# Performance work log

Measured on AMD Instinct MI355X. Metric: run time of the kernel, lower is better.

Reference implementation:

```python
import jax, jax.numpy as jnp
import numpy as np

N_NODES = 100000
N_EDGES = 1600000
D_NODE = 32
D_EDGE = 16
D_OUT = 32
L2_EPS = 1e-12  # tf.math.l2_normalize default epsilon


def setup_inputs() -> dict:
    key = jax.random.key(0)
    k_h, k_e, k_w, k_s, k_d = jax.random.split(key, 5)
    h = jax.random.normal(k_h, (N_NODES, D_NODE), dtype=jnp.float32)
    e = jax.random.normal(k_e, (N_EDGES, D_EDGE), dtype=jnp.float32)
    # Dense(output_dim) kernel over concat(node, edge) features
    W = jax.random.normal(k_w, (D_NODE + D_EDGE, D_OUT), dtype=jnp.float32) * 0.1
    b = jnp.zeros((D_OUT,), dtype=jnp.float32)
    src = jax.random.randint(k_s, (N_EDGES,), 0, N_NODES, dtype=jnp.int32)
    dst = jax.random.randint(k_d, (N_EDGES,), 0, N_NODES, dtype=jnp.int32)
    return {"h": h, "e": e, "W": W, "b": b, "src": src, "dst": dst}


def reference(h, e, W, b, src, dst):
    # message: m = concat(h[src], e)              [E, D+De]
    # reduce:  new_h = mean over (self_msg, mailbox) of Dense(msg)
    # Dense is affine (activation=None), so Dense(mean) == mean(Dense): one GEMM.
    n = h.shape[0]
    msg = jnp.concatenate([h[src], e], axis=-1)                      # [E, D+De]
    agg = jax.ops.segment_sum(msg, dst, num_segments=n)              # [N, D+De]
    deg = jax.ops.segment_sum(jnp.ones_like(dst, dtype=h.dtype), dst, num_segments=n)
    self_msg = jnp.concatenate([h, jnp.zeros((n, e.shape[1]), h.dtype)], axis=-1)
    mean_msg = (self_msg + agg) / (deg[:, None] + 1.0)               # self counts in the mean
    new_h = mean_msg @ W + b                                         # [N, D_OUT]
    # activation=None -> identity; then tf.math.l2_normalize(axis=-1)
    sq = jnp.sum(new_h * new_h, axis=-1, keepdims=True)
    return new_h * jax.lax.rsqrt(jnp.maximum(sq, L2_EPS))
```

## Files before the change

kernel.cpp:

```cpp
#include <hip/hip_runtime.h>

#define D_NODE 32
#define D_EDGE 16
#define D_IN   48
#define D_OUT  32
#define L2_EPS 1e-12f

#define NPB       64
#define BKT_SHIFT 6
#define MAX_NB    4096
#define CH        8192
#define CTH       1024
#define EPT       (CH / CTH)
#define ATH       256
#define CAP       2048
#define KPT       (CAP / ATH)


__global__ __launch_bounds__(CTH) void k_count(
    const int* __restrict__ dst, int* __restrict__ cnt, int n_edges, int nb)
{
    extern __shared__ int c[];
    for (int i = threadIdx.x; i < nb; i += CTH) c[i] = 0;
    __syncthreads();
    int base = blockIdx.x * CH + threadIdx.x;
    #pragma unroll
    for (int k = 0; k < EPT; ++k) {
        int i = base + k * CTH;
        if (i < n_edges) atomicAdd(&c[dst[i] >> BKT_SHIFT], 1);
    }
    __syncthreads();
    for (int i = threadIdx.x; i < nb; i += CTH)
        if (c[i]) atomicAdd(&cnt[i], c[i]);
}

__global__ __launch_bounds__(1024) void k_offs2(
    const int* __restrict__ cnt, int* __restrict__ offsets,
    int* __restrict__ cursor, int nb)
{
    __shared__ int s[1024];
    const int PT = MAX_NB / 1024;
    int t = threadIdx.x;
    int tot[PT];
    int ts = 0;
    #pragma unroll
    for (int j = 0; j < PT; ++j) {
        int b = t * PT + j;
        tot[j] = (b < nb) ? cnt[b] : 0;
        ts += tot[j];
    }
    s[t] = ts;
    __syncthreads();
    for (int off = 1; off < 1024; off <<= 1) {
        int u = (t >= off) ? s[t - off] : 0;
        __syncthreads();
        s[t] += u;
        __syncthreads();
    }
    if (t == 1023) offsets[nb] = s[1023];
    int run = s[t] - ts;
    #pragma unroll
    for (int j = 0; j < PT; ++j) {
        int b = t * PT + j;
        if (b < nb) { offsets[b] = run; cursor[b] = run; run += tot[j]; }
    }
}

__global__ __launch_bounds__(CTH) void k_scatter3(
    const int* __restrict__ dst, const int* __restrict__ src,
    int* __restrict__ cursor, int2* __restrict__ meta2, int n_edges, int nb)
{
    extern __shared__ int sm[];
    int* lhist = sm;
    int* lbase = sm + nb;
    int* lrank = sm + 2 * nb;
    for (int i = threadIdx.x; i < nb; i += CTH) { lhist[i] = 0; lrank[i] = 0; }
    __syncthreads();
    int base = blockIdx.x * CH + threadIdx.x;
    int d[EPT];
    #pragma unroll
    for (int k = 0; k < EPT; ++k) {
        int i = base + k * CTH;
        if (i < n_edges) {
            d[k] = dst[i];
            atomicAdd(&lhist[d[k] >> BKT_SHIFT], 1);
        }
    }
    __syncthreads();
    for (int i = threadIdx.x; i < nb; i += CTH)
        if (lhist[i]) lbase[i] = atomicAdd(&cursor[i], lhist[i]);
    __syncthreads();
    #pragma unroll
    for (int k = 0; k < EPT; ++k) {
        int i = base + k * CTH;
        if (i < n_edges) {
            int bkt = d[k] >> BKT_SHIFT;
            int r = atomicAdd(&lrank[bkt], 1);
            meta2[lbase[bkt] + r] =
                make_int2(src[i] | ((d[k] & (NPB - 1)) << 20), i);
        }
    }
}

__global__ __launch_bounds__(ATH, 8) void k_accum(
    const float* __restrict__ h, const float4* __restrict__ e4,
    const float* __restrict__ W, const float* __restrict__ b,
    const int* __restrict__ offsets, const int2* __restrict__ meta2,
    float* __restrict__ out, int n_nodes)
{
    __shared__ float Ws[D_IN * D_OUT];
    __shared__ float bs[D_OUT];
    __shared__ int2 csr[CAP];
    __shared__ int cnt[NPB], cnt2[NPB], offs[NPB];

    for (int i = threadIdx.x; i < D_IN * D_OUT; i += ATH) Ws[i] = W[i];
    if (threadIdx.x < D_OUT) bs[threadIdx.x] = b[threadIdx.x];
    if (threadIdx.x < NPB) { cnt[threadIdx.x] = 0; cnt2[threadIdx.x] = 0; }
    __syncthreads();

    int g  = threadIdx.x >> 2;
    int jg = threadIdx.x & 3;

    float4 ha0 = make_float4(0.f, 0.f, 0.f, 0.f);
    float4 ha1 = make_float4(0.f, 0.f, 0.f, 0.f);
    float4 ea  = make_float4(0.f, 0.f, 0.f, 0.f);
    float deg = 0.f;

    int b0 = offsets[blockIdx.x], b1 = offsets[blockIdx.x + 1];

    for (int t0 = b0; t0 < b1; t0 += CAP) {
        int tn = min(CAP, b1 - t0);

        int2 m[KPT];
        #pragma unroll
        for (int k = 0; k < KPT; ++k) {
            int i = (int)threadIdx.x + k * ATH;
            if (i < tn) {
                m[k] = meta2[t0 + i];
                atomicAdd(&cnt[(m[k].x >> 20) & (NPB - 1)], 1);
            }
        }
        __syncthreads();

        if (threadIdx.x < 64) {
            int p = cnt[threadIdx.x];
            int x = p;
            #pragma unroll
            for (int o = 1; o < 64; o <<= 1) {
                int y = __shfl_up(x, o);
                if (threadIdx.x >= o) x += y;
            }
            offs[threadIdx.x] = x - p;
        }
        int myc = cnt[g];
        __syncthreads();

        #pragma unroll
        for (int k = 0; k < KPT; ++k) {
            int i = (int)threadIdx.x + k * ATH;
            if (i < tn) {
                int dl = (m[k].x >> 20) & (NPB - 1);
                int r = atomicAdd(&cnt2[dl], 1);
                csr[offs[dl] + r] = make_int2(m[k].x & 0xFFFFF, m[k].y);
            }
        }
        if (threadIdx.x < NPB) cnt[threadIdx.x] = 0;
        deg += (float)myc;
        __syncthreads();

        int mybase = offs[g];
        #pragma unroll 4
        for (int s = 0; s < myc; ++s) {
            int2 c = csr[mybase + s];
            const float4* hr = reinterpret_cast<const float4*>(
                h + (size_t)c.x * D_NODE) + 2 * jg;
            float4 h0 = hr[0], h1 = hr[1];
            float4 ev = e4[(size_t)c.y * 4 + jg];
            ha0.x += h0.x; ha0.y += h0.y; ha0.z += h0.z; ha0.w += h0.w;
            ha1.x += h1.x; ha1.y += h1.y; ha1.z += h1.z; ha1.w += h1.w;
            ea.x  += ev.x; ea.y  += ev.y; ea.z  += ev.z; ea.w  += ev.w;
        }
        if (threadIdx.x < NPB) cnt2[threadIdx.x] = 0;
        __syncthreads();
    }

    float (*mrow)[D_IN + 1] = reinterpret_cast<float (*)[D_IN + 1]>(csr);

    int node = blockIdx.x * NPB + g;
    if (node < n_nodes) {
        float inv = 1.f / (deg + 1.f);
        const float4* hs = reinterpret_cast<const float4*>(
            h + (size_t)node * D_NODE) + 2 * jg;
        float4 s0 = hs[0], s1 = hs[1];
        mrow[g][8 * jg + 0] = (ha0.x + s0.x) * inv;
        mrow[g][8 * jg + 1] = (ha0.y + s0.y) * inv;
        mrow[g][8 * jg + 2] = (ha0.z + s0.z) * inv;
        mrow[g][8 * jg + 3] = (ha0.w + s0.w) * inv;
        mrow[g][8 * jg + 4] = (ha1.x + s1.x) * inv;
        mrow[g][8 * jg + 5] = (ha1.y + s1.y) * inv;
        mrow[g][8 * jg + 6] = (ha1.z + s1.z) * inv;
        mrow[g][8 * jg + 7] = (ha1.w + s1.w) * inv;
        mrow[g][D_NODE + 4 * jg + 0] = ea.x * inv;
        mrow[g][D_NODE + 4 * jg + 1] = ea.y * inv;
        mrow[g][D_NODE + 4 * jg + 2] = ea.z * inv;
        mrow[g][D_NODE + 4 * jg + 3] = ea.w * inv;
    }
    __syncthreads();
    if (node >= n_nodes) return;

    const float* row = mrow[g];
    float a[8];
    #pragma unroll
    for (int q = 0; q < 8; ++q) a[q] = bs[jg * 8 + q];
    #pragma unroll
    for (int k = 0; k < D_IN; ++k) {
        float mk = row[k];
        const float* w = Ws + k * D_OUT + jg * 8;
        #pragma unroll
        for (int q = 0; q < 8; ++q) a[q] += mk * w[q];
    }
    float sq = 0.f;
    #pragma unroll
    for (int q = 0; q < 8; ++q) sq += a[q] * a[q];
    sq += __shfl_xor(sq, 1);
    sq += __shfl_xor(sq, 2);
    float r = rsqrtf(fmaxf(sq, L2_EPS));
    float4* o4 = reinterpret_cast<float4*>(out + (size_t)node * D_OUT) + 2 * jg;
    o4[0] = make_float4(a[0] * r, a[1] * r, a[2] * r, a[3] * r);
    o4[1] = make_float4(a[4] * r, a[5] * r, a[6] * r, a[7] * r);
}

__global__ __launch_bounds__(256) void scatter_kernel(
    const float* __restrict__ h, const float* __restrict__ e,
    const int* __restrict__ src, const int* __restrict__ dst,
    float* __restrict__ agg, float* __restrict__ deg, int n_edges)
{
    int tid  = blockIdx.x * blockDim.x + threadIdx.x;
    int edge = tid >> 4;
    int c    = tid & 15;
    if (edge >= n_edges) return;
    int s = src[edge], d = dst[edge];
    float v0 = h[(size_t)s * D_NODE + c];
    float v1 = h[(size_t)s * D_NODE + 16 + c];
    float v2 = e[(size_t)edge * D_EDGE + c];
    float* row = agg + (size_t)d * D_IN;
    atomicAdd(row + c, v0);
    atomicAdd(row + 16 + c, v1);
    atomicAdd(row + 32 + c, v2);
    if (c == 0) atomicAdd(deg + d, 1.0f);
}

__global__ __launch_bounds__(256) void node_kernel(
    const float* __restrict__ h, const float* __restrict__ W, const float* __restrict__ b,
    const float* __restrict__ agg, const float* __restrict__ deg,
    float* __restrict__ out, int n_nodes)
{
    __shared__ float Ws[D_IN * D_OUT];
    __shared__ float bs[D_OUT];
    for (int i = threadIdx.x; i < D_IN * D_OUT; i += blockDim.x) Ws[i] = W[i];
    if (threadIdx.x < D_OUT) bs[threadIdx.x] = b[threadIdx.x];
    __syncthreads();
    int node = blockIdx.x * blockDim.x + threadIdx.x;
    if (node >= n_nodes) return;
    const float4* h4 = reinterpret_cast<const float4*>(h + (size_t)node * D_NODE);
    const float4* a4 = reinterpret_cast<const float4*>(agg + (size_t)node * D_IN);
    float inv = 1.0f / (deg[node] + 1.0f);
    float m[D_IN];
    #pragma unroll
    for (int k = 0; k < D_NODE / 4; ++k) {
        float4 hv = h4[k]; float4 av = a4[k];
        m[4*k+0] = (hv.x + av.x) * inv; m[4*k+1] = (hv.y + av.y) * inv;
        m[4*k+2] = (hv.z + av.z) * inv; m[4*k+3] = (hv.w + av.w) * inv;
    }
    #pragma unroll
    for (int k = D_NODE / 4; k < D_IN / 4; ++k) {
        float4 av = a4[k];
        m[4*k+0] = av.x * inv; m[4*k+1] = av.y * inv;
        m[4*k+2] = av.z * inv; m[4*k+3] = av.w * inv;
    }
    float acc[D_OUT];
    #pragma unroll
    for (int j = 0; j < D_OUT; ++j) acc[j] = bs[j];
    #pragma unroll
    for (int k = 0; k < D_IN; ++k) {
        float mk = m[k];
        #pragma unroll
        for (int j = 0; j < D_OUT; ++j) acc[j] += mk * Ws[k * D_OUT + j];
    }
    float sq = 0.0f;
    #pragma unroll
    for (int j = 0; j < D_OUT; ++j) sq += acc[j] * acc[j];
    float r = rsqrtf(fmaxf(sq, L2_EPS));
    float4* o4 = reinterpret_cast<float4*>(out + (size_t)node * D_OUT);
    #pragma unroll
    for (int j = 0; j < D_OUT / 4; ++j) {
        float4 v;
        v.x = acc[4*j+0] * r; v.y = acc[4*j+1] * r;
        v.z = acc[4*j+2] * r; v.w = acc[4*j+3] * r;
        o4[j] = v;
    }
}

extern "C" void kernel_launch(void* const* d_in, const int* in_sizes, int n_in,
                              void* d_out, int out_size, void* d_ws, size_t ws_size,
                              hipStream_t stream) {
    const float* h   = (const float*)d_in[0];
    const float* e   = (const float*)d_in[1];
    const float* W   = (const float*)d_in[2];
    const float* b   = (const float*)d_in[3];
    const int*   src = (const int*)d_in[4];
    const int*   dst = (const int*)d_in[5];
    float* out = (float*)d_out;

    const int n_nodes = in_sizes[0] / D_NODE;
    const int n_edges = in_sizes[4];

    const int nb = (n_nodes + NPB - 1) / NPB;
    const int nc = (n_edges + CH - 1) / CH;

    size_t o_cnt     = 0;
    size_t o_offsets = o_cnt + nb;
    size_t o_cursor  = o_offsets + nb + 1;
    size_t o_meta2   = (o_cursor + (size_t)nb + 1) & ~(size_t)1;
    size_t need      = (o_meta2 + (size_t)n_edges * 2) * sizeof(int);

    if (nb <= MAX_NB && n_nodes < (1 << 20) && need <= ws_size && n_edges > 0) {
        int* ws_i    = (int*)d_ws;
        int* cnt     = ws_i + o_cnt;
        int* offsets = ws_i + o_offsets;
        int* cursor  = ws_i + o_cursor;
        int2* meta2  = (int2*)(ws_i + o_meta2);

        hipMemsetAsync(cnt, 0, (size_t)nb * sizeof(int), stream);
        k_count<<<nc, CTH, (size_t)nb * sizeof(int), stream>>>(
            dst, cnt, n_edges, nb);
        k_offs2<<<1, 1024, 0, stream>>>(cnt, offsets, cursor, nb);
        k_scatter3<<<nc, CTH, (size_t)3 * nb * sizeof(int), stream>>>(
            dst, src, cursor, meta2, n_edges, nb);
        k_accum<<<nb, ATH, 0, stream>>>(
            h, (const float4*)e, W, b, offsets, meta2, out, n_nodes);
    } else {
        float* agg = (float*)d_ws;
        float* deg = agg + (size_t)n_nodes * D_IN;
        hipMemsetAsync(d_ws, 0, (size_t)n_nodes * (D_IN + 1) * sizeof(float), stream);
        long long threads = (long long)n_edges * 16;
        scatter_kernel<<<(int)((threads + 255) / 256), 256, 0, stream>>>(h, e, src, dst, agg, deg, n_edges);
        node_kernel<<<(n_nodes + 255) / 256, 256, 0, stream>>>(h, W, b, agg, deg, out, n_nodes);
    }
}
```

Measured before the change: 116.2 us.

## Permute edge features into bucket order during scatter for contiguous reads

The scatter pass now copies each edge's 16-float feature row into a bucket-sorted buffer alongside a compact 4-byte meta word, rather than writing an (src,edge_id) pair. The accumulate kernel then reads edge features from that bucket-contiguous buffer instead of gathering them randomly from the original array. This swaps random 64-byte gathers for a streaming read, at the cost of an extra scattered 64-byte write per edge and about 100MB of extra workspace. The previous path is kept as a fallback when the workspace is too small.

```diff
diff --git a/kernel.cpp b/kernel.cpp
--- a/kernel.cpp
+++ b/kernel.cpp
@@ -66,7 +66,49 @@
     }
 }
 
-__global__ __launch_bounds__(CTH) void k_scatter3(
+__global__ __launch_bounds__(CTH) void k_scatter_p(
+    const int* __restrict__ dst, const int* __restrict__ src,
+    int* __restrict__ cursor, int* __restrict__ meta1,
+    float4* __restrict__ ep, const float4* __restrict__ e4,
+    int n_edges, int nb)
+{
+    extern __shared__ int sm[];
+    int* lhist = sm;
+    int* lbase = sm + nb;
+    int* lrank = sm + 2 * nb;
+    for (int i = threadIdx.x; i < nb; i += CTH) { lhist[i] = 0; lrank[i] = 0; }
+    __syncthreads();
+    int base = blockIdx.x * CH + threadIdx.x;
+    int d[EPT];
+    #pragma unroll
+    for (int k = 0; k < EPT; ++k) {
+        int i = base + k * CTH;
+        if (i < n_edges) {
+            d[k] = dst[i];
+            atomicAdd(&lhist[d[k] >> BKT_SHIFT], 1);
+        }
+    }
+    __syncthreads();
+    for (int i = threadIdx.x; i < nb; i += CTH)
+        if (lhist[i]) lbase[i] = atomicAdd(&cursor[i], lhist[i]);
+    __syncthreads();
+    #pragma unroll
+    for (int k = 0; k < EPT; ++k) {
+        int i = base + k * CTH;
+        if (i < n_edges) {
+            int bkt = d[k] >> BKT_SHIFT;
+            int r = atomicAdd(&lrank[bkt], 1);
+            int slot = lbase[bkt] + r;
+            meta1[slot] = src[i] | ((d[k] & (NPB - 1)) << 20);
+            const float4* er = e4 + (size_t)i * 4;
+            float4 v0 = er[0], v1 = er[1], v2 = er[2], v3 = er[3];
+            float4* wp = ep + (size_t)slot * 4;
+            wp[0] = v0; wp[1] = v1; wp[2] = v2; wp[3] = v3;
+        }
+    }
+}
+
+__global__ __launch_bounds__(CTH) void k_scatter_g(
     const int* __restrict__ dst, const int* __restrict__ src,
     int* __restrict__ cursor, int2* __restrict__ meta2, int n_edges, int nb)
 {
@@ -102,10 +144,10 @@
     }
 }
 
-__global__ __launch_bounds__(ATH, 8) void k_accum(
-    const float* __restrict__ h, const float4* __restrict__ e4,
+__global__ __launch_bounds__(ATH, 8) void k_accum_p(
+    const float* __restrict__ h, const float4* __restrict__ ep,
     const float* __restrict__ W, const float* __restrict__ b,
-    const int* __restrict__ offsets, const int2* __restrict__ meta2,
+    const int* __restrict__ offsets, const int* __restrict__ meta1,
     float* __restrict__ out, int n_nodes)
 {
     __shared__ float Ws[D_IN * D_OUT];
@@ -131,13 +173,13 @@
     for (int t0 = b0; t0 < b1; t0 += CAP) {
         int tn = min(CAP, b1 - t0);
 
-        int2 m[KPT];
+        int m[KPT];
         #pragma unroll
         for (int k = 0; k < KPT; ++k) {
             int i = (int)threadIdx.x + k * ATH;
             if (i < tn) {
-                m[k] = meta2[t0 + i];
-                atomicAdd(&cnt[(m[k].x >> 20) & (NPB - 1)], 1);
+                m[k] = meta1[t0 + i];
+                atomicAdd(&cnt[(m[k] >> 20) & (NPB - 1)], 1);
             }
         }
         __syncthreads();
@@ -159,9 +201,9 @@
         for (int k = 0; k < KPT; ++k) {
             int i = (int)threadIdx.x + k * ATH;
             if (i < tn) {
-                int dl = (m[k].x >> 20) & (NPB - 1);
+                int dl = (m[k] >> 20) & (NPB - 1);
                 int r = atomicAdd(&cnt2[dl], 1);
-                csr[offs[dl] + r] = make_int2(m[k].x & 0xFFFFF, m[k].y);
+                csr[offs[dl] + r] = make_int2(m[k] & 0xFFFFF, i);
             }
         }
         if (threadIdx.x < NPB) cnt[threadIdx.x] = 0;
@@ -175,7 +217,7 @@
             const float4* hr = reinterpret_cast<const float4*>(
                 h + (size_t)c.x * D_NODE) + 2 * jg;
             float4 h0 = hr[0], h1 = hr[1];
-            float4 ev = e4[(size_t)c.y * 4 + jg];
+            float4 ev = ep[(size_t)(t0 + c.y) * 4 + jg];
             ha0.x += h0.x; ha0.y += h0.y; ha0.z += h0.z; ha0.w += h0.w;
             ha1.x += h1.x; ha1.y += h1.y; ha1.z += h1.z; ha1.w += h1.w;
             ea.x  += ev.x; ea.y  += ev.y; ea.z  += ev.z; ea.w  += ev.w;
@@ -230,6 +272,134 @@
     o4[1] = make_float4(a[4] * r, a[5] * r, a[6] * r, a[7] * r);
 }
 
+__global__ __launch_bounds__(ATH, 8) void k_accum_g(
+    const float* __restrict__ h, const float4* __restrict__ e4,
+    const float* __restrict__ W, const float* __restrict__ b,
+    const int* __restrict__ offsets, const int2* __restrict__ meta2,
+    float* __restrict__ out, int n_nodes)
+{
+    __shared__ float Ws[D_IN * D_OUT];
+    __shared__ float bs[D_OUT];
+    __shared__ int2 csr[CAP];
+    __shared__ int cnt[NPB], cnt2[NPB], offs[NPB];
+
+    for (int i = threadIdx.x; i < D_IN * D_OUT; i += ATH) Ws[i] = W[i];
+    if (threadIdx.x < D_OUT) bs[threadIdx.x] = b[threadIdx.x];
+    if (threadIdx.x < NPB) { cnt[threadIdx.x] = 0; cnt2[threadIdx.x] = 0; }
+    __syncthreads();
+
+    int g  = threadIdx.x >> 2;
+    int jg = threadIdx.x & 3;
+
+    float4 ha0 = make_float4(0.f, 0.f, 0.f, 0.f);
+    float4 ha1 = make_float4(0.f, 0.f, 0.f, 0.f);
+    float4 ea  = make_float4(0.f, 0.f, 0.f, 0.f);
+    float deg = 0.f;
+
+    int b0 = offsets[blockIdx.x], b1 = offsets[blockIdx.x + 1];
+
+    for (int t0 = b0; t0 < b1; t0 += CAP) {
+        int tn = min(CAP, b1 - t0);
+
+        int2 m[KPT];
+        #pragma unroll
+        for (int k = 0; k < KPT; ++k) {
+            int i = (int)threadIdx.x + k * ATH;
+            if (i < tn) {
+                m[k] = meta2[t0 + i];
+                atomicAdd(&cnt[(m[k].x >> 20) & (NPB - 1)], 1);
+            }
+        }
+        __syncthreads();
+
+        if (threadIdx.x < 64) {
+            int p = cnt[threadIdx.x];
+            int x = p;
+            #pragma unroll
+            for (int o = 1; o < 64; o <<= 1) {
+                int y = __shfl_up(x, o);
+                if (threadIdx.x >= o) x += y;
+            }
+            offs[threadIdx.x] = x - p;
+        }
+        int myc = cnt[g];
+        __syncthreads();
+
+        #pragma unroll
+        for (int k = 0; k < KPT; ++k) {
+            int i = (int)threadIdx.x + k * ATH;
+            if (i < tn) {
+                int dl = (m[k].x >> 20) & (NPB - 1);
+                int r = atomicAdd(&cnt2[dl], 1);
+                csr[offs[dl] + r] = make_int2(m[k].x & 0xFFFFF, m[k].y);
+            }
+        }
+        if (threadIdx.x < NPB) cnt[threadIdx.x] = 0;
+        deg += (float)myc;
+        __syncthreads();
+
+        int mybase = offs[g];
+        #pragma unroll 4
+        for (int s = 0; s < myc; ++s) {
+            int2 c = csr[mybase + s];
+            const float4* hr = reinterpret_cast<const float4*>(
+                h + (size_t)c.x * D_NODE) + 2 * jg;
+            float4 h0 = hr[0], h1 = hr[1];
+            float4 ev = e4[(size_t)c.y * 4 + jg];
+            ha0.x += h0.x; ha0.y += h0.y; ha0.z += h0.z; ha0.w += h0.w;
+            ha1.x += h1.x; ha1.y += h1.y; ha1.z += h1.z; ha1.w += h1.w;
+            ea.x  += ev.x; ea.y  += ev.y; ea.z  += ev.z; ea.w  += ev.w;
+        }
+        if (threadIdx.x < NPB) cnt2[threadIdx.x] = 0;
+        __syncthreads();
+    }
+
+    float (*mrow)[D_IN + 1] = reinterpret_cast<float (*)[D_IN + 1]>(csr);
+
+    int node = blockIdx.x * NPB + g;
+    if (node < n_nodes) {
+        float inv = 1.f / (deg + 1.f);
+        const float4* hs = reinterpret_cast<const float4*>(
+            h + (size_t)node * D_NODE) + 2 * jg;
+        float4 s0 = hs[0], s1 = hs[1];
+        mrow[g][8 * jg + 0] = (ha0.x + s0.x) * inv;
+        mrow[g][8 * jg + 1] = (ha0.y + s0.y) * inv;
+        mrow[g][8 * jg + 2] = (ha0.z + s0.z) * inv;
+        mrow[g][8 * jg + 3] = (ha0.w + s0.w) * inv;
+        mrow[g][8 * jg + 4] = (ha1.x + s1.x) * inv;
+        mrow[g][8 * jg + 5] = (ha1.y + s1.y) * inv;
+        mrow[g][8 * jg + 6] = (ha1.z + s1.z) * inv;
+        mrow[g][8 * jg + 7] = (ha1.w + s1.w) * inv;
+        mrow[g][D_NODE + 4 * jg + 0] = ea.x * inv;
+        mrow[g][D_NODE + 4 * jg + 1] = ea.y * inv;
+        mrow[g][D_NODE + 4 * jg + 2] = ea.z * inv;
+        mrow[g][D_NODE + 4 * jg + 3] = ea.w * inv;
+    }
+    __syncthreads();
+    if (node >= n_nodes) return;
+
+    const float* row = mrow[g];
+    float a[8];
+    #pragma unroll
+    for (int q = 0; q < 8; ++q) a[q] = bs[jg * 8 + q];
+    #pragma unroll
+    for (int k = 0; k < D_IN; ++k) {
+        float mk = row[k];
+        const float* w = Ws + k * D_OUT + jg * 8;
+        #pragma unroll
+        for (int q = 0; q < 8; ++q) a[q] += mk * w[q];
+    }
+    float sq = 0.f;
+    #pragma unroll
+    for (int q = 0; q < 8; ++q) sq += a[q] * a[q];
+    sq += __shfl_xor(sq, 1);
+    sq += __shfl_xor(sq, 2);
+    float r = rsqrtf(fmaxf(sq, L2_EPS));
+    float4* o4 = reinterpret_cast<float4*>(out + (size_t)node * D_OUT) + 2 * jg;
+    o4[0] = make_float4(a[0] * r, a[1] * r, a[2] * r, a[3] * r);
+    o4[1] = make_float4(a[4] * r, a[5] * r, a[6] * r, a[7] * r);
+}
+
 __global__ __launch_bounds__(256) void scatter_kernel(
     const float* __restrict__ h, const float* __restrict__ e,
     const int* __restrict__ src, const int* __restrict__ dst,
@@ -321,10 +491,34 @@
     size_t o_cnt     = 0;
     size_t o_offsets = o_cnt + nb;
     size_t o_cursor  = o_offsets + nb + 1;
-    size_t o_meta2   = (o_cursor + (size_t)nb + 1) & ~(size_t)1;
-    size_t need      = (o_meta2 + (size_t)n_edges * 2) * sizeof(int);
-
-    if (nb <= MAX_NB && n_nodes < (1 << 20) && need <= ws_size && n_edges > 0) {
+    size_t o_hdr_end = o_cursor + nb;
+
+    size_t o_meta1 = o_hdr_end;
+    size_t o_ep    = (o_meta1 + (size_t)n_edges + 3) & ~(size_t)3;
+    size_t need_A  = (o_ep + (size_t)n_edges * 16) * sizeof(int);
+
+    size_t o_meta2 = (o_hdr_end + 1) & ~(size_t)1;
+    size_t need_B  = (o_meta2 + (size_t)n_edges * 2) * sizeof(int);
+
+    bool ok_common = (nb <= MAX_NB) && (n_nodes < (1 << 20)) && (n_edges > 0);
+
+    if (ok_common && need_A <= ws_size) {
+        int* ws_i    = (int*)d_ws;
+        int* cnt     = ws_i + o_cnt;
+        int* offsets = ws_i + o_offsets;
+        int* cursor  = ws_i + o_cursor;
+        int* meta1   = ws_i + o_meta1;
+        float4* ep   = (float4*)(ws_i + o_ep);
+
+        hipMemsetAsync(cnt, 0, (size_t)nb * sizeof(int), stream);
+        k_count<<<nc, CTH, (size_t)nb * sizeof(int), stream>>>(
+            dst, cnt, n_edges, nb);
+        k_offs2<<<1, 1024, 0, stream>>>(cnt, offsets, cursor, nb);
+        k_scatter_p<<<nc, CTH, (size_t)3 * nb * sizeof(int), stream>>>(
+            dst, src, cursor, meta1, ep, (const float4*)e, n_edges, nb);
+        k_accum_p<<<nb, ATH, 0, stream>>>(
+            h, (const float4*)ep, W, b, offsets, meta1, out, n_nodes);
+    } else if (ok_common && need_B <= ws_size) {
         int* ws_i    = (int*)d_ws;
         int* cnt     = ws_i + o_cnt;
         int* offsets = ws_i + o_offsets;
@@ -335,9 +529,9 @@
         k_count<<<nc, CTH, (size_t)nb * sizeof(int), stream>>>(
             dst, cnt, n_edges, nb);
         k_offs2<<<1, 1024, 0, stream>>>(cnt, offsets, cursor, nb);
-        k_scatter3<<<nc, CTH, (size_t)3 * nb * sizeof(int), stream>>>(
+        k_scatter_g<<<nc, CTH, (size_t)3 * nb * sizeof(int), stream>>>(
             dst, src, cursor, meta2, n_edges, nb);
-        k_accum<<<nb, ATH, 0, stream>>>(
+        k_accum_g<<<nb, ATH, 0, stream>>>(
             h, (const float4*)e, W, b, offsets, meta2, out, n_nodes);
     } else {
         float* agg = (float*)d_ws;
```

New measurement: 220.6 us. +89.8%, slower.
